# Optimization experiments

Hardware: AMD Instinct MI355X
Metric: run time of the kernel (lower is better)

Reference implementation:

```python
import jax, jax.numpy as jnp
import numpy as np

SR = 48000.0  # sample_rate from init_kwargs


def setup_inputs() -> dict:
    key = jax.random.key(0)
    k1, = jax.random.split(key, 1)
    B, T = 32, 480000  # 10 seconds of 48 kHz audio, batch of 32
    x = jax.random.normal(k1, (B, T), dtype=jnp.float32)
    t = jnp.zeros((B,), dtype=jnp.float32)  # unused by the module's forward
    filter_freq = jnp.array([15000.0], dtype=jnp.float32)  # learnable param
    filter_q = jnp.array([0.9], dtype=jnp.float32)         # learnable param
    return {"x": x, "t": t, "filter_freq": filter_freq, "filter_q": filter_q}


def _biquad_coeffs(filter_freq, filter_q):
    # torchaudio.functional.lowpass_biquad coefficient computation
    f = jnp.clip(filter_freq[0], 100.0, SR / 2 - 1)
    q = jnp.clip(filter_q[0], 0.1, 10.0)
    w0 = 2.0 * jnp.pi * f / SR
    alpha = jnp.sin(w0) / (2.0 * q)
    cosw = jnp.cos(w0)
    b0 = (1.0 - cosw) / 2.0
    b1 = 1.0 - cosw
    b2 = b0
    a0 = 1.0 + alpha
    a1 = -2.0 * cosw
    a2 = 1.0 - alpha
    # torchaudio normalizes all coefficients by a0
    return b0 / a0, b1 / a0, b2 / a0, a1 / a0, a2 / a0


def reference(x, t, filter_freq, filter_q):
    # x: [B, T]. Direct-form-I biquad recurrence along time, zero initial state:
    b0, b1, b2, a1, a2 = _biquad_coeffs(filter_freq, filter_q)

    def step(carry, xt):
        x1, x2, y1, y2 = carry  # each [B]
        y = b0 * xt + b1 * x1 + b2 * x2 - a1 * y1 - a2 * y2
        return (xt, x1, y, y1), y

    z = jnp.zeros(x.shape[0], dtype=x.dtype)
    _, ys = jax.lax.scan(step, (z, z, z, z), x.T)  # scan over time: [T, B]
    return ys.T  # [B, T]
```

## Files before the change

kernel.cpp:

```cpp
#include <hip/hip_runtime.h>


#define SR_F      48000.0f
#define T_LEN     480000
#define B_ROWS    32
#define CHUNK     32
#define WARM      32
#define BLOCK     256
#define TILE      (BLOCK * CHUNK)
#define NBLOCKS   ((B_ROWS * T_LEN) / TILE)
#define CHUNKS_PER_ROW (T_LEN / CHUNK)
#define GSTRIDE   33

__global__ __launch_bounds__(BLOCK) void biquad_lds(
    const float* __restrict__ x,
    const float* __restrict__ ffreq,
    const float* __restrict__ fqual,
    float* __restrict__ out)
{
    __shared__ float tile[BLOCK * GSTRIDE];
    __shared__ float halo[WARM];

    const int t = threadIdx.x;
    const size_t tile_start = (size_t)blockIdx.x * TILE;

    float f = fminf(fmaxf(ffreq[0], 100.0f), SR_F * 0.5f - 1.0f);
    float q = fminf(fmaxf(fqual[0], 0.1f), 10.0f);
    float w0 = 2.0f * 3.14159265358979323846f * f / SR_F;
    float alpha = sinf(w0) / (2.0f * q);
    float cw = cosf(w0);
    float inv_a0 = 1.0f / (1.0f + alpha);
    const float b0c = (1.0f - cw) * 0.5f * inv_a0;
    const float b1c = (1.0f - cw) * inv_a0;
    const float b2c = b0c;
    const float a1c = (-2.0f * cw) * inv_a0;
    const float a2c = (1.0f - alpha) * inv_a0;

    {
        const float4* gx = (const float4*)(x + tile_start);
        #pragma unroll
        for (int j = 0; j < TILE / 4 / BLOCK; ++j) {
            float4 v = gx[t + BLOCK * j];
            int p = 4 * (t + BLOCK * j);
            float* dst = &tile[(p >> 5) * GSTRIDE + (p & 31)];
            dst[0] = v.x; dst[1] = v.y; dst[2] = v.z; dst[3] = v.w;
        }
        if (t < WARM / 4 && blockIdx.x != 0) {
            float4 v = *(const float4*)(x + tile_start - WARM + 4 * t);
            halo[4*t] = v.x; halo[4*t+1] = v.y; halo[4*t+2] = v.z; halo[4*t+3] = v.w;
        }
    }
    __syncthreads();

    const int chunk_id = blockIdx.x * BLOCK + t;
    const bool row_start = (chunk_id % CHUNKS_PER_ROW) == 0;

    float x1 = 0.0f, x2 = 0.0f, y1 = 0.0f, y2 = 0.0f;

    if (!row_start) {
        const float* ws = (t == 0) ? halo : &tile[(t - 1) * GSTRIDE];
        #pragma unroll
        for (int i = 0; i < WARM; ++i) {
            float xi = ws[i];
            float v = fmaf(b1c, x1, b0c * xi);
            v = fmaf(b2c, x2, v);
            v = fmaf(-a2c, y2, v);
            v = fmaf(-a1c, y1, v);
            x2 = x1; x1 = xi; y2 = y1; y1 = v;
        }
    }
    __syncthreads();

    {
        float* ms = &tile[t * GSTRIDE];
        #pragma unroll
        for (int i = 0; i < CHUNK; ++i) {
            float xi = ms[i];
            float v = fmaf(b1c, x1, b0c * xi);
            v = fmaf(b2c, x2, v);
            v = fmaf(-a2c, y2, v);
            v = fmaf(-a1c, y1, v);
            ms[i] = v;
            x2 = x1; x1 = xi; y2 = y1; y1 = v;
        }
    }
    __syncthreads();

    {
        float4* gy = (float4*)(out + tile_start);
        #pragma unroll
        for (int j = 0; j < TILE / 4 / BLOCK; ++j) {
            int p = 4 * (t + BLOCK * j);
            const float* src = &tile[(p >> 5) * GSTRIDE + (p & 31)];
            gy[t + BLOCK * j] = make_float4(src[0], src[1], src[2], src[3]);
        }
    }
}

extern "C" void kernel_launch(void* const* d_in, const int* in_sizes, int n_in,
                              void* d_out, int out_size, void* d_ws, size_t ws_size,
                              hipStream_t stream)
{
    const float* x  = (const float*)d_in[0];
    const float* ff = (const float*)d_in[2];
    const float* fq = (const float*)d_in[3];
    float* out = (float*)d_out;

    biquad_lds<<<NBLOCKS, BLOCK, 0, stream>>>(x, ff, fq, out);
}
```

Measured before the change: 111.5 us.

## Use direct global-to-LDS loads with XOR-swizzled float4 tile and larger chunks

```diff
diff --git a/kernel.cpp b/kernel.cpp
--- a/kernel.cpp
+++ b/kernel.cpp
@@ -1,16 +1,22 @@
 #include <hip/hip_runtime.h>
+#include <stdint.h>
 
 
 #define SR_F      48000.0f
 #define T_LEN     480000
 #define B_ROWS    32
-#define CHUNK     32
+#define CHUNK     64
 #define WARM      32
-#define BLOCK     256
+#define BLOCK     128
 #define TILE      (BLOCK * CHUNK)
+#define TILE_F4   (TILE / 4)
 #define NBLOCKS   ((B_ROWS * T_LEN) / TILE)
 #define CHUNKS_PER_ROW (T_LEN / CHUNK)
-#define GSTRIDE   33
+
+typedef const __attribute__((address_space(1))) uint32_t gbl_u32;
+typedef __attribute__((address_space(3))) uint32_t lds_u32;
+
+__device__ __forceinline__ int swz(int qi) { return qi ^ ((qi >> 4) & 7); }
 
 __global__ __launch_bounds__(BLOCK) void biquad_lds(
     const float* __restrict__ x,
@@ -18,16 +24,15 @@
     const float* __restrict__ fqual,
     float* __restrict__ out)
 {
-    __shared__ float tile[BLOCK * GSTRIDE];
-    __shared__ float halo[WARM];
+    __shared__ float4 tile4[TILE_F4];
+    __shared__ float4 halo4[WARM / 4];
 
     const int t = threadIdx.x;
-    const size_t tile_start = (size_t)blockIdx.x * TILE;
 
     float f = fminf(fmaxf(ffreq[0], 100.0f), SR_F * 0.5f - 1.0f);
-    float q = fminf(fmaxf(fqual[0], 0.1f), 10.0f);
+    float qq = fminf(fmaxf(fqual[0], 0.1f), 10.0f);
     float w0 = 2.0f * 3.14159265358979323846f * f / SR_F;
-    float alpha = sinf(w0) / (2.0f * q);
+    float alpha = sinf(w0) / (2.0f * qq);
     float cw = cosf(w0);
     float inv_a0 = 1.0f / (1.0f + alpha);
     const float b0c = (1.0f - cw) * 0.5f * inv_a0;
@@ -36,18 +41,23 @@
     const float a1c = (-2.0f * cw) * inv_a0;
     const float a2c = (1.0f - alpha) * inv_a0;
 
+    const size_t tile_f4_start = (size_t)blockIdx.x * TILE_F4;
+    const float4* gx = (const float4*)x + tile_f4_start;
+
     {
-        const float4* gx = (const float4*)(x + tile_start);
+        const int qw = __builtin_amdgcn_readfirstlane(t & 64);
+        const int ln = t & 63;
         #pragma unroll
-        for (int j = 0; j < TILE / 4 / BLOCK; ++j) {
-            float4 v = gx[t + BLOCK * j];
-            int p = 4 * (t + BLOCK * j);
-            float* dst = &tile[(p >> 5) * GSTRIDE + (p & 31)];
-            dst[0] = v.x; dst[1] = v.y; dst[2] = v.z; dst[3] = v.w;
+        for (int j = 0; j < TILE_F4 / BLOCK; ++j) {
+            int qbase = j * BLOCK + qw;
+            __builtin_amdgcn_global_load_lds(
+                (gbl_u32*)&gx[swz(qbase + ln)],
+                (lds_u32*)&tile4[qbase], 16, 0, 0);
         }
-        if (t < WARM / 4 && blockIdx.x != 0) {
-            float4 v = *(const float4*)(x + tile_start - WARM + 4 * t);
-            halo[4*t] = v.x; halo[4*t+1] = v.y; halo[4*t+2] = v.z; halo[4*t+3] = v.w;
+        if (blockIdx.x != 0 && t < WARM / 4) {
+            const float4* gh = (const float4*)x + tile_f4_start - WARM / 4;
+            __builtin_amdgcn_global_load_lds(
+                (gbl_u32*)&gh[t], (lds_u32*)&halo4[0], 16, 0, 0);
         }
     }
     __syncthreads();
@@ -57,44 +67,47 @@
 
     float x1 = 0.0f, x2 = 0.0f, y1 = 0.0f, y2 = 0.0f;
 
+#define STEP(xi, yo) do {                       \
+        float v_ = fmaf(b1c, x1, b0c * (xi));   \
+        v_ = fmaf(b2c, x2, v_);                 \
+        v_ = fmaf(-a2c, y2, v_);                \
+        v_ = fmaf(-a1c, y1, v_);                \
+        x2 = x1; x1 = (xi); y2 = y1; y1 = v_;   \
+        (yo) = v_;                              \
+    } while (0)
+
     if (!row_start) {
-        const float* ws = (t == 0) ? halo : &tile[(t - 1) * GSTRIDE];
+        float sink;
         #pragma unroll
-        for (int i = 0; i < WARM; ++i) {
-            float xi = ws[i];
-            float v = fmaf(b1c, x1, b0c * xi);
-            v = fmaf(b2c, x2, v);
-            v = fmaf(-a2c, y2, v);
-            v = fmaf(-a1c, y1, v);
-            x2 = x1; x1 = xi; y2 = y1; y1 = v;
+        for (int k = 0; k < WARM / 4; ++k) {
+            float4 v = (t == 0) ? halo4[k] : tile4[swz(16 * t - 8 + k)];
+            STEP(v.x, sink); STEP(v.y, sink); STEP(v.z, sink); STEP(v.w, sink);
+        }
+        (void)sink;
+    }
+    __syncthreads();
+
+    {
+        #pragma unroll
+        for (int k = 0; k < CHUNK / 4; ++k) {
+            int qi = swz(16 * t + k);
+            float4 v = tile4[qi];
+            float4 o;
+            STEP(v.x, o.x); STEP(v.y, o.y); STEP(v.z, o.z); STEP(v.w, o.w);
+            tile4[qi] = o;
         }
     }
     __syncthreads();
 
     {
-        float* ms = &tile[t * GSTRIDE];
+        float4* gy = (float4*)out + tile_f4_start;
         #pragma unroll
-        for (int i = 0; i < CHUNK; ++i) {
-            float xi = ms[i];
-            float v = fmaf(b1c, x1, b0c * xi);
-            v = fmaf(b2c, x2, v);
-            v = fmaf(-a2c, y2, v);
-            v = fmaf(-a1c, y1, v);
-            ms[i] = v;
-            x2 = x1; x1 = xi; y2 = y1; y1 = v;
+        for (int j = 0; j < TILE_F4 / BLOCK; ++j) {
+            int qv = t + BLOCK * j;
+            gy[qv] = tile4[swz(qv)];
         }
     }
-    __syncthreads();
-
-    {
-        float4* gy = (float4*)(out + tile_start);
-        #pragma unroll
-        for (int j = 0; j < TILE / 4 / BLOCK; ++j) {
-            int p = 4 * (t + BLOCK * j);
-            const float* src = &tile[(p >> 5) * GSTRIDE + (p & 31)];
-            gy[t + BLOCK * j] = make_float4(src[0], src[1], src[2], src[3]);
-        }
-    }
+#undef STEP
 }
 
 extern "C" void kernel_launch(void* const* d_in, const int* in_sizes, int n_in,
```

Result: no change. 111.7 us (+0.1%).
